# Kernel tuning notes

Hardware: AMD Instinct MI355X
Metric: run time of the kernel (lower is better)

## Reference

```python
import jax, jax.numpy as jnp
import numpy as np

D_MODEL = 1024
N_QK = 32
D_QK = 32
N_OV = 2048
D_OV = 1
SEQ = 1024
BATCH = 2
VKV = 16
ROT_DIM = 32
ROT_BASE = 10000.0
SCALE = D_QK ** 0.5  # cfg.attn_scale default = sqrt(d_qk_head)


def _kaiming(k, shape, fan_in):
    # torch kaiming_normal_(mode='fan_in', nonlinearity='relu'): std = sqrt(2/fan_in)
    return jax.random.normal(k, shape, jnp.float32) * np.sqrt(2.0 / fan_in)


def setup_inputs() -> dict:
    key = jax.random.key(0)
    ks = jax.random.split(key, 7)
    return {
        'resid': jax.random.normal(ks[0], (BATCH, SEQ, D_MODEL), jnp.float32),
        'W_Q': _kaiming(ks[1], (N_QK, D_MODEL, D_QK), D_MODEL * D_QK),
        'W_K': _kaiming(ks[2], (N_QK, D_MODEL, D_QK), D_MODEL * D_QK),
        'W_V': _kaiming(ks[3], (N_OV, D_MODEL, D_OV), D_MODEL * D_OV),
        'W_O': _kaiming(ks[4], (N_OV, D_OV, D_MODEL), D_OV * D_MODEL),
        'b_Q': jnp.zeros((N_QK, D_QK), jnp.float32),
        'b_K': jnp.zeros((N_QK, D_QK), jnp.float32),
        'b_V': jnp.zeros((N_OV, D_OV), jnp.float32),
        'virtual_k': _kaiming(ks[5], (VKV, N_QK, D_QK), N_QK * D_QK),
        'virtual_v': jnp.zeros((VKV, N_OV, D_OV), jnp.float32),
    }


def _rotary_sin_cos(n_ctx, rd, base):
    # GPT-NeoX style (non-adjacent pairs): freq repeated as (2 d)
    pos = jnp.arange(n_ctx, dtype=jnp.float32)
    dim = jnp.arange(rd // 2, dtype=jnp.float32)
    freq = base ** (dim / (rd / 2))
    freq = jnp.concatenate([freq, freq])
    angles = pos[:, None] / freq[None, :]  # (n_ctx, rd)
    return jnp.sin(angles), jnp.cos(angles)


def _apply_rotary(x, sin, cos, rd):
    # x: (batch, seq, head, d_head)
    s = x.shape[1]
    x_rot, x_pass = x[..., :rd], x[..., rd:]
    flip = jnp.concatenate([-x_rot[..., rd // 2:], x_rot[..., :rd // 2]], axis=-1)
    rot = x_rot * cos[None, :s, None, :] + flip * sin[None, :s, None, :]
    return jnp.concatenate([rot, x_pass], axis=-1)


def reference(resid, W_Q, W_K, W_V, W_O, b_Q, b_K, b_V, virtual_k, virtual_v):
    b, s, _ = resid.shape
    # per-head QKV projections + biases
    q = jnp.einsum('bsm,hmd->bshd', resid, W_Q) + b_Q  # (b,s,n_qk,d_qk)
    k = jnp.einsum('bsm,hmd->bshd', resid, W_K) + b_K
    v = jnp.einsum('bsm,hmd->bshd', resid, W_V) + b_V  # (b,s,n_ov,d_ov)
    sin, cos = _rotary_sin_cos(s, ROT_DIM, ROT_BASE)
    q = _apply_rotary(q, sin, cos, ROT_DIM)
    k = _apply_rotary(k, sin, cos, ROT_DIM)
    # append virtual KV at the end of the key axis
    k = jnp.concatenate([k, jnp.broadcast_to(virtual_k[None], (b,) + virtual_k.shape)], axis=1)
    v = jnp.concatenate([v, jnp.broadcast_to(virtual_v[None], (b,) + virtual_v.shape)], axis=1)
    kv_len = s + VKV
    scores = jnp.einsum('bqhd,bkhd->bhqk', q, k) / SCALE
    # causal mask: tril(ones(n_ctx, n_ctx+vkv), diagonal=vkv)
    mask = jnp.arange(kv_len)[None, :] <= (jnp.arange(s)[:, None] + VKV)
    scores = jnp.where(mask[None, None], scores, -jnp.inf)
    pattern = jax.nn.softmax(scores, axis=-1)
    pattern = jnp.where(jnp.isnan(pattern), 0.0, pattern)
    # repeat_interleave of pattern over ov heads == grouping v per qk head
    ratio = N_OV // N_QK
    v_g = v.reshape(b, kv_len, N_QK, ratio * D_OV)
    z = jnp.einsum('bhqk,bkhr->bqhr', pattern, v_g)  # (b,s,n_qk,ratio*d_ov)
    z = z.reshape(b, s, N_OV, D_OV)
    out = jnp.einsum('bqhd,hdm->bqm', z, W_O)  # cal_out: no b_O
    return out
```

## Files before the change

kernel.cpp:

```cpp
#include <hip/hip_runtime.h>
#include <hip/hip_bf16.h>
#include <math.h>


typedef short bf16x8 __attribute__((ext_vector_type(8)));
typedef short short4v __attribute__((ext_vector_type(4)));
typedef float f32x4 __attribute__((ext_vector_type(4)));
typedef int int4v __attribute__((ext_vector_type(4)));
typedef __hip_bfloat16 bf16;

#define AS1(p) ((const __attribute__((address_space(1))) void*)(const void*)(p))
#define AS3(p) ((__attribute__((address_space(3))) void*)(void*)(p))

static constexpr float INV_SCALE = 0.17677669529663687f;

__device__ inline short rnd_bf16(float x) {
  unsigned u = __float_as_uint(x);
  return (short)((u + 0x7fffu + ((u >> 16) & 1u)) >> 16);
}

__device__ inline int pack_bf16_pair(float hi, float lo) {
  unsigned a = __float_as_uint(hi) + 0x8000u;
  unsigned b = __float_as_uint(lo) + 0x8000u;
  return (int)__builtin_amdgcn_perm(a, b, 0x07060302u);
}

__global__ __launch_bounds__(256) void prep(
    const float* __restrict__ resid, const float* __restrict__ WV,
    const float* __restrict__ WQ, const float* __restrict__ WK,
    const float* __restrict__ WO, const float* __restrict__ vk,
    const float* __restrict__ vv,
    bf16* __restrict__ A_bf, bf16* __restrict__ Wt, bf16* __restrict__ Wot,
    bf16* __restrict__ Kb, bf16* __restrict__ Vb) {
  __shared__ float t[64][65];
  const int blk = blockIdx.x, tid = threadIdx.x;
  if (blk < 4096) {
    const float* src = (blk < 2048) ? resid : WV;
    short* dst = (short*)((blk < 2048) ? A_bf : (Wt + (size_t)2048 * 1024));
    int i = ((blk & 2047) * 256 + tid) * 4;
    float4 v = *(const float4*)(src + i);
    dst[i + 0] = rnd_bf16(v.x); dst[i + 1] = rnd_bf16(v.y);
    dst[i + 2] = rnd_bf16(v.z); dst[i + 3] = rnd_bf16(v.w);
  } else if (blk < 7168) {
    int idx = (blk - 4096) * 256 + tid;
    if (idx < 262144) {
      int b = idx >> 17, rem = idx & 131071;
      int j = rem >> 10, c = rem & 1023;
      int h = c >> 5, d = c & 31;
      float v = (j < 16) ? vk[j * 1024 + c] : 0.f;
      Kb[(((size_t)(b * 32 + h)) * 1152 + 1024 + j) * 32 + d] = __float2bfloat16(v);
    } else if (idx < 524288) {
      int i2 = idx - 262144;
      int b = i2 >> 17, rem = i2 & 131071;
      int ch = rem >> 6, p = rem & 63;
      int pl = p & 31;
      int u = (p & 32) | ((pl & 4) << 2) | ((pl & 24) >> 1) | (pl & 3);
      float v = (u < 16) ? vv[(size_t)u * 2048 + ch] : 0.f;
      int hv = ch >> 6, c = ch & 63;
      int slot = c * 8 + ((p >> 3) ^ (c & 7));
      Vb[((((size_t)(b * 32 + hv)) * 17 + 16) * 512 + slot) * 8 + (p & 7)] = __float2bfloat16(v);
    }
  } else if (blk < 8192) {
    int i = blk - 7168;
    int mt = i & 15, h = (i >> 4) & 31, qk = i >> 9;
    const float* W = qk ? WK : WQ;
    const int m0 = mt * 64;
    for (int idx = tid; idx < 64 * 32; idx += 256) {
      int ii = idx >> 5, d = idx & 31;
      t[ii][d] = W[((size_t)h * 1024 + m0 + ii) * 32 + d];
    }
    __syncthreads();
    const int rowbase = qk * 1024 + h * 32;
    for (int idx = tid; idx < 32 * 64; idx += 256) {
      int d = idx >> 6, ii = idx & 63;
      Wt[(size_t)(rowbase + d) * 1024 + m0 + ii] = __float2bfloat16(t[ii][d]);
    }
  } else {
    int i = blk - 8192;
    int h0 = (i & 31) * 64, m0 = (i >> 5) * 64;
    for (int idx = tid; idx < 64 * 64; idx += 256) {
      int ii = idx >> 6, j = idx & 63;
      t[ii][j] = WO[(size_t)(h0 + ii) * 1024 + m0 + j];
    }
    __syncthreads();
    for (int idx = tid; idx < 64 * 64; idx += 256) {
      int ii = idx >> 6, j = idx & 63;
      Wot[(size_t)(m0 + ii) * 2048 + h0 + j] = __float2bfloat16(t[j][ii]);
    }
  }
}

__global__ __launch_bounds__(256) void gemm1_fused(
    const bf16* __restrict__ A, const bf16* __restrict__ Bt,
    const float* __restrict__ bQ, const float* __restrict__ bK,
    const float* __restrict__ bV,
    bf16* __restrict__ Qb, bf16* __restrict__ Kb, bf16* __restrict__ Vb) {
  __shared__ __align__(16) short As[128 * 64];
  __shared__ __align__(16) short Bs[128 * 64];
  const int flat = blockIdx.x;
  const int xcd = flat & 7, idx = flat >> 3;
  const int tileM = (xcd * 2 + (idx >> 5)) * 128;
  const int tileN = (idx & 31) * 128;
  const int tid = threadIdx.x, wave = tid >> 6, lane = tid & 63;
  const int wm = (wave >> 1) * 64, wn = (wave & 1) * 64;
  const int mrow = lane & 15, kq = lane >> 4;
  const bool isQK = tileN < 2048;
  f32x4 acc[4][4] = {};

  for (int k0 = 0; k0 < 1024; k0 += 64) {
#pragma unroll
    for (int i = 0; i < 4; i++) {
      int c = (wave * 4 + i) * 64 + lane;
      int row = c >> 3, j = c & 7, g = j ^ (row & 7);
      const short* ga = (const short*)A + (size_t)(tileM + row) * 1024 + k0 + g * 8;
      const short* gb = (const short*)Bt + (size_t)(tileN + row) * 1024 + k0 + g * 8;
      __builtin_amdgcn_global_load_lds(AS1(ga), AS3(&As[(wave * 4 + i) * 512]), 16, 0, 0);
      __builtin_amdgcn_global_load_lds(AS1(gb), AS3(&Bs[(wave * 4 + i) * 512]), 16, 0, 0);
    }
    __syncthreads();
#pragma unroll
    for (int ks = 0; ks < 2; ks++) {
      bf16x8 af[4], bfr[4];
#pragma unroll
      for (int t = 0; t < 4; t++) {
        int ra = wm + t * 16 + mrow, rb = wn + t * 16 + mrow;
        af[t]  = *(const bf16x8*)&As[ra * 64 + ((ks * 4 + kq) ^ (ra & 7)) * 8];
        bfr[t] = *(const bf16x8*)&Bs[rb * 64 + ((ks * 4 + kq) ^ (rb & 7)) * 8];
      }
      if (isQK) {
#pragma unroll
        for (int fj = 0; fj < 4; fj++)
#pragma unroll
          for (int ti = 0; ti < 4; ti++)
            acc[fj][ti] = __builtin_amdgcn_mfma_f32_16x16x32_bf16(bfr[fj], af[ti], acc[fj][ti], 0, 0, 0);
      } else {
#pragma unroll
        for (int i = 0; i < 4; i++)
#pragma unroll
          for (int j = 0; j < 4; j++)
            acc[i][j] = __builtin_amdgcn_mfma_f32_16x16x32_bf16(af[i], bfr[j], acc[i][j], 0, 0, 0);
      }
    }
    __syncthreads();
  }

  const int col = lane & 15, rq = lane >> 4;
  if (isQK) {
    const int qk = tileN >> 10;
    const float* bias = qk ? bK : bQ;
    const int hA = ((tileN & 1023) + wn) >> 5;
    const int d0 = rq * 4;
    const float4 bA0 = *(const float4*)&bias[hA * 32 + d0];
    const float4 bA1 = *(const float4*)&bias[hA * 32 + 16 + d0];
    const float4 bB0 = *(const float4*)&bias[(hA + 1) * 32 + d0];
    const float4 bB1 = *(const float4*)&bias[(hA + 1) * 32 + 16 + d0];
    float invf[4];
#pragma unroll
    for (int r = 0; r < 4; r++)
      invf[r] = exp2f((d0 + r) * -0.8304820237218406f);
    const float osc = qk ? 1.f : INV_SCALE;
#pragma unroll
    for (int ti = 0; ti < 4; ti++) {
      int sg = tileM + wm + ti * 16 + col;
      int s = sg & 1023, bb = sg >> 10;
      float sv[4], cv[4];
#pragma unroll
      for (int r = 0; r < 4; r++) __sincosf((float)s * invf[r], &sv[r], &cv[r]);
#pragma unroll
      for (int p = 0; p < 2; p++) {
        int h = hA + p;
        short4v z0, z1;
#pragma unroll
        for (int r = 0; r < 4; r++) {
          float x0 = acc[2 * p][ti][r]     + (p ? (&bB0.x)[r] : (&bA0.x)[r]);
          float x1 = acc[2 * p + 1][ti][r] + (p ? (&bB1.x)[r] : (&bA1.x)[r]);
          float y0 = (x0 * cv[r] - x1 * sv[r]) * osc;
          float y1 = (x1 * cv[r] + x0 * sv[r]) * osc;
          z0[r] = rnd_bf16(y0); z1[r] = rnd_bf16(y1);
        }
        short* dst = qk
            ? (short*)Kb + ((size_t)(bb * 32 + h) * 1152 + s) * 32
            : (short*)Qb + ((size_t)(bb * 32 + h) * 1024 + s) * 32;
        *(short4v*)(dst + d0) = z0;
        *(short4v*)(dst + 16 + d0) = z1;
      }
    }
  } else {
    const int hv = (tileN - 2048 + wn) >> 6;
#pragma unroll
    for (int i = 0; i < 4; i++)
#pragma unroll
      for (int j = 0; j < 4; j++) {
        int c = j * 16 + col;
        float bias = bV[hv * 64 + c];
        int m0 = tileM + wm + i * 16 + rq * 4;
        int s0 = m0 & 1023, bb = m0 >> 10;
        int chunk = s0 >> 6, w = s0 & 63, u0 = w & 31;
        int p0 = (u0 & 3) | ((u0 & 16) >> 2) | ((u0 & 8) << 1) | ((u0 & 4) << 1);
        int p = (w & 32) | p0;
        int slot = c * 8 + ((p >> 3) ^ (c & 7));
        short4v s4;
#pragma unroll
        for (int r = 0; r < 4; r++) s4[r] = rnd_bf16(acc[i][j][r] + bias);
        *(short4v*)((short*)Vb +
            ((((size_t)(bb * 32 + hv)) * 17 + chunk) * 512 + slot) * 8 + (p & 7)) = s4;
      }
  }
}

__global__ __launch_bounds__(256) void attn_mfma(
    const bf16* __restrict__ Qb, const bf16* __restrict__ Kb,
    const bf16* __restrict__ Vb, bf16* __restrict__ Zb) {
  __shared__ __align__(16) short Vs[4][2][4096];
  const int flat = blockIdx.x;
  const int xcd = flat & 7;
  const int hqb = xcd * 8 + ((flat >> 3) & 7);
  const int xblk = flat >> 6;
  const int hq = hqb & 31, b = hqb >> 5;
  const int wave = threadIdx.x >> 6, lane = threadIdx.x & 63;
  const int col = lane & 15, quad = lane >> 4;
  const int pairIdx = xblk * 4 + wave;
  const int qwA = pairIdx * 16, qwB = (63 - pairIdx) * 16;

  const short* qbase = (const short*)Qb + ((size_t)(b * 32 + hq)) * 1024 * 32;
  const bf16x8 qfA = *(const bf16x8*)(qbase + (qwA + col) * 32 + quad * 8);
  const bf16x8 qfB = *(const bf16x8*)(qbase + (qwB + col) * 32 + quad * 8);
  const short* kbase = (const short*)Kb + ((size_t)(b * 32 + hq)) * 1152 * 32 + quad * 8;
  const short* vbh = (const short*)Vb + ((size_t)(b * 32 + hq)) * (17 * 4096) + lane * 8;

  const int kendA = qwA + 32;
  const int nchA = (kendA + 63) >> 6;
  const int kendB = (qwB + 32 < 1040) ? qwB + 32 : 1040;
  const int nchB = (kendB + 63) >> 6;

  f32x4 OA[4] = {}, OB[4] = {};
  float mA = -1e30f, lA = 0.f, mB = -1e30f, lB = 0.f;

  bf16x8 kf[4];
#pragma unroll
  for (int mbk = 0; mbk < 4; mbk++)
    kf[mbk] = *(const bf16x8*)(kbase + (size_t)(mbk * 16 + col) * 32);
  {
    short* vd = &Vs[wave][0][0];
#pragma unroll
    for (int g = 0; g < 8; g++)
      __builtin_amdgcn_global_load_lds(AS1(vbh + g * 512), AS3(vd + g * 512), 16, 0, 0);
  }

  for (int ci = 0; ci < nchB; ci++) {
    const int kc = ci * 64;
    const bool aAct = ci < nchA;
    f32x4 SB[4] = {};
#pragma unroll
    for (int mbk = 0; mbk < 4; mbk++)
      SB[mbk] = __builtin_amdgcn_mfma_f32_16x16x32_bf16(kf[mbk], qfB, SB[mbk], 0, 0, 0);
    f32x4 SA[4] = {};
    if (aAct) {
#pragma unroll
      for (int mbk = 0; mbk < 4; mbk++)
        SA[mbk] = __builtin_amdgcn_mfma_f32_16x16x32_bf16(kf[mbk], qfA, SA[mbk], 0, 0, 0);
    }
    if (kc + 63 > qwB + 16) {
      int qv = qwB + col + 16;
#pragma unroll
      for (int mbk = 0; mbk < 4; mbk++)
#pragma unroll
        for (int r = 0; r < 4; r++)
          if (kc + mbk * 16 + quad * 4 + r > qv) SB[mbk][r] = -1e30f;
    }
    if (aAct && kc + 63 > qwA + 16) {
      int qv = qwA + col + 16;
#pragma unroll
      for (int mbk = 0; mbk < 4; mbk++)
#pragma unroll
        for (int r = 0; r < 4; r++)
          if (kc + mbk * 16 + quad * 4 + r > qv) SA[mbk][r] = -1e30f;
    }
    int4v piB[2], piA[2];
    {
      float c0 = fmaxf(fmaxf(SB[0][0], SB[0][1]), fmaxf(SB[0][2], SB[0][3]));
      float c1 = fmaxf(fmaxf(SB[1][0], SB[1][1]), fmaxf(SB[1][2], SB[1][3]));
      float c2 = fmaxf(fmaxf(SB[2][0], SB[2][1]), fmaxf(SB[2][2], SB[2][3]));
      float c3 = fmaxf(fmaxf(SB[3][0], SB[3][1]), fmaxf(SB[3][2], SB[3][3]));
      float cmax = fmaxf(fmaxf(c0, c1), fmaxf(c2, c3));
      cmax = fmaxf(cmax, __shfl_xor(cmax, 16));
      cmax = fmaxf(cmax, __shfl_xor(cmax, 32));
      float mn = fmaxf(mB, cmax);
      float al = __expf(mB - mn);
      mB = mn;
      float ps = 0.f;
#pragma unroll
      for (int mbk = 0; mbk < 4; mbk++)
#pragma unroll
        for (int r = 0; r < 4; r++) {
          float p = __expf(SB[mbk][r] - mn);
          ps += p;
          SB[mbk][r] = p;
        }
      ps += __shfl_xor(ps, 16);
      ps += __shfl_xor(ps, 32);
      lB = lB * al + ps;
#pragma unroll
      for (int pr = 0; pr < 2; pr++)
#pragma unroll
        for (int d = 0; d < 4; d++)
          piB[pr][d] = pack_bf16_pair(SB[2 * pr + (d >> 1)][(d & 1) * 2 + 1],
                                      SB[2 * pr + (d >> 1)][(d & 1) * 2]);
#pragma unroll
      for (int cb = 0; cb < 4; cb++)
#pragma unroll
        for (int r = 0; r < 4; r++) OB[cb][r] *= al;
    }
    if (aAct) {
      float c0 = fmaxf(fmaxf(SA[0][0], SA[0][1]), fmaxf(SA[0][2], SA[0][3]));
      float c1 = fmaxf(fmaxf(SA[1][0], SA[1][1]), fmaxf(SA[1][2], SA[1][3]));
      float c2 = fmaxf(fmaxf(SA[2][0], SA[2][1]), fmaxf(SA[2][2], SA[2][3]));
      float c3 = fmaxf(fmaxf(SA[3][0], SA[3][1]), fmaxf(SA[3][2], SA[3][3]));
      float cmax = fmaxf(fmaxf(c0, c1), fmaxf(c2, c3));
      cmax = fmaxf(cmax, __shfl_xor(cmax, 16));
      cmax = fmaxf(cmax, __shfl_xor(cmax, 32));
      float mn = fmaxf(mA, cmax);
      float al = __expf(mA - mn);
      mA = mn;
      float ps = 0.f;
#pragma unroll
      for (int mbk = 0; mbk < 4; mbk++)
#pragma unroll
        for (int r = 0; r < 4; r++) {
          float p = __expf(SA[mbk][r] - mn);
          ps += p;
          SA[mbk][r] = p;
        }
      ps += __shfl_xor(ps, 16);
      ps += __shfl_xor(ps, 32);
      lA = lA * al + ps;
#pragma unroll
      for (int pr = 0; pr < 2; pr++)
#pragma unroll
        for (int d = 0; d < 4; d++)
          piA[pr][d] = pack_bf16_pair(SA[2 * pr + (d >> 1)][(d & 1) * 2 + 1],
                                      SA[2 * pr + (d >> 1)][(d & 1) * 2]);
#pragma unroll
      for (int cb = 0; cb < 4; cb++)
#pragma unroll
        for (int r = 0; r < 4; r++) OA[cb][r] *= al;
    }
    asm volatile("s_waitcnt vmcnt(0)" ::: "memory");
    const short* vd = &Vs[wave][ci & 1][0];
    bf16x8 vf[2][4];
#pragma unroll
    for (int ks = 0; ks < 2; ks++)
#pragma unroll
      for (int cb = 0; cb < 4; cb++) {
        int slot = (cb * 16 + col) * 8 + ((ks * 4 + quad) ^ (col & 7));
        vf[ks][cb] = *(const bf16x8*)(vd + slot * 8);
      }
    if (ci + 1 < nchB) {
      const int kn = kc + 64;
#pragma unroll
      for (int mbk = 0; mbk < 4; mbk++)
        kf[mbk] = *(const bf16x8*)(kbase + (size_t)(kn + mbk * 16 + col) * 32);
      const short* vsrc = vbh + (ci + 1) * 4096;
      short* vdn = &Vs[wave][(ci + 1) & 1][0];
#pragma unroll
      for (int g = 0; g < 8; g++)
        __builtin_amdgcn_global_load_lds(AS1(vsrc + g * 512), AS3(vdn + g * 512), 16, 0, 0);
    }
#pragma unroll
    for (int ks = 0; ks < 2; ks++) {
      bf16x8 prB = *(bf16x8*)&piB[ks];
#pragma unroll
      for (int cb = 0; cb < 4; cb++)
        OB[cb] = __builtin_amdgcn_mfma_f32_16x16x32_bf16(vf[ks][cb], prB, OB[cb], 0, 0, 0);
    }
    if (aAct) {
#pragma unroll
      for (int ks = 0; ks < 2; ks++) {
        bf16x8 prA = *(bf16x8*)&piA[ks];
#pragma unroll
        for (int cb = 0; cb < 4; cb++)
          OA[cb] = __builtin_amdgcn_mfma_f32_16x16x32_bf16(vf[ks][cb], prA, OA[cb], 0, 0, 0);
      }
    }
  }
  {
    float inv = 1.f / lA;
    short* zrow = (short*)Zb + ((size_t)(b * 1024 + qwA + col)) * 2048 + hq * 64 + quad * 4;
#pragma unroll
    for (int cb = 0; cb < 4; cb++) {
      short4v s4;
#pragma unroll
      for (int r = 0; r < 4; r++) s4[r] = rnd_bf16(OA[cb][r] * inv);
      *(short4v*)(zrow + cb * 16) = s4;
    }
  }
  {
    float inv = 1.f / lB;
    short* zrow = (short*)Zb + ((size_t)(b * 1024 + qwB + col)) * 2048 + hq * 64 + quad * 4;
#pragma unroll
    for (int cb = 0; cb < 4; cb++) {
      short4v s4;
#pragma unroll
      for (int r = 0; r < 4; r++) s4[r] = rnd_bf16(OB[cb][r] * inv);
      *(short4v*)(zrow + cb * 16) = s4;
    }
  }
}

__global__ __launch_bounds__(256) void gemm2_small(
    const bf16* __restrict__ A, const bf16* __restrict__ Bt, float* __restrict__ C,
    int K, int ldc) {
  __shared__ __align__(16) short As[64 * 128];
  __shared__ __align__(16) short Bs[64 * 128];
  const int tileM = blockIdx.y * 64, tileN = blockIdx.x * 64;
  const int tid = threadIdx.x, wave = tid >> 6, lane = tid & 63;
  const int wm = (wave >> 1) * 32, wn = (wave & 1) * 32;
  const int mrow = lane & 15, kq = lane >> 4;
  f32x4 acc[2][2] = {};

  for (int k0 = 0; k0 < K; k0 += 128) {
#pragma unroll
    for (int i = 0; i < 4; i++) {
      int c = (wave * 4 + i) * 64 + lane;
      int row = c >> 4, j = c & 15, g = j ^ (row & 15);
      const short* ga = (const short*)A + (size_t)(tileM + row) * K + k0 + g * 8;
      const short* gb = (const short*)Bt + (size_t)(tileN + row) * K + k0 + g * 8;
      __builtin_amdgcn_global_load_lds(AS1(ga), AS3(&As[(wave * 4 + i) * 512]), 16, 0, 0);
      __builtin_amdgcn_global_load_lds(AS1(gb), AS3(&Bs[(wave * 4 + i) * 512]), 16, 0, 0);
    }
    __syncthreads();
#pragma unroll
    for (int ks = 0; ks < 4; ks++) {
      bf16x8 af[2], bfr[2];
#pragma unroll
      for (int t = 0; t < 2; t++) {
        int ra = wm + t * 16 + mrow, rb = wn + t * 16 + mrow;
        af[t]  = *(const bf16x8*)&As[ra * 128 + ((ks * 4 + kq) ^ (ra & 15)) * 8];
        bfr[t] = *(const bf16x8*)&Bs[rb * 128 + ((ks * 4 + kq) ^ (rb & 15)) * 8];
      }
#pragma unroll
      for (int i = 0; i < 2; i++)
#pragma unroll
        for (int j = 0; j < 2; j++)
          acc[i][j] = __builtin_amdgcn_mfma_f32_16x16x32_bf16(af[i], bfr[j], acc[i][j], 0, 0, 0);
    }
    __syncthreads();
  }
  const int col = lane & 15, rq = lane >> 4;
#pragma unroll
  for (int i = 0; i < 2; i++)
#pragma unroll
    for (int j = 0; j < 2; j++)
#pragma unroll
      for (int r = 0; r < 4; r++) {
        int mm = tileM + wm + i * 16 + rq * 4 + r;
        int nn = tileN + wn + j * 16 + col;
        C[(size_t)mm * ldc + nn] = acc[i][j][r];
      }
}

extern "C" void kernel_launch(void* const* d_in, const int* in_sizes, int n_in,
                              void* d_out, int out_size, void* d_ws, size_t ws_size,
                              hipStream_t stream) {
  const float* resid = (const float*)d_in[0];
  const float* WQ = (const float*)d_in[1];
  const float* WK = (const float*)d_in[2];
  const float* WV = (const float*)d_in[3];
  const float* WO = (const float*)d_in[4];
  const float* bQ = (const float*)d_in[5];
  const float* bK = (const float*)d_in[6];
  const float* bV = (const float*)d_in[7];
  const float* vk = (const float*)d_in[8];
  const float* vv = (const float*)d_in[9];
  float* out = (float*)d_out;

  char* ws = (char*)d_ws;
  bf16* A_bf = (bf16*)(ws);
  bf16* Wt   = (bf16*)(ws + 4194304);
  bf16* Wot  = (bf16*)(ws + 12582912);
  bf16* Qb   = (bf16*)(ws + 16777216);
  bf16* Kb   = (bf16*)(ws + 20971520);
  bf16* Vb   = (bf16*)(ws + 25690112);
  bf16* Zb   = (bf16*)(ws + 35127296);

  prep<<<8704, 256, 0, stream>>>(resid, WV, WQ, WK, WO, vk, vv, A_bf, Wt, Wot, Kb, Vb);
  gemm1_fused<<<512, 256, 0, stream>>>(A_bf, Wt, bQ, bK, bV, Qb, Kb, Vb);
  attn_mfma<<<512, 256, 0, stream>>>(Qb, Kb, Vb, Zb);
  gemm2_small<<<dim3(16, 32), 256, 0, stream>>>(Zb, Wot, out, 2048, 1024);
}
```

Measured before the change: 160.1 us.

## Double-buffer LDS tiles in output GEMM and reorder attention block scheduling

The output-projection GEMM now keeps two LDS buffers, so the global-to-LDS loads for the next K tile are issued before the MFMA work on the current tile. This is meant to hide global memory latency behind compute, at the cost of doubling LDS use, which may lower occupancy. Separately, the attention kernel remaps block indices above 3 in reverse order, changing which query-pair blocks are dispatched together to balance the causal workload.

```diff
diff --git a/kernel.cpp b/kernel.cpp
--- a/kernel.cpp
+++ b/kernel.cpp
@@ -215,7 +215,8 @@
   const int flat = blockIdx.x;
   const int xcd = flat & 7;
   const int hqb = xcd * 8 + ((flat >> 3) & 7);
-  const int xblk = flat >> 6;
+  const int xb = flat >> 6;
+  const int xblk = (xb < 4) ? xb : (11 - xb);
   const int hq = hqb & 31, b = hqb >> 5;
   const int wave = threadIdx.x >> 6, lane = threadIdx.x & 63;
   const int col = lane & 15, quad = lane >> 4;
@@ -410,33 +411,45 @@
 __global__ __launch_bounds__(256) void gemm2_small(
     const bf16* __restrict__ A, const bf16* __restrict__ Bt, float* __restrict__ C,
     int K, int ldc) {
-  __shared__ __align__(16) short As[64 * 128];
-  __shared__ __align__(16) short Bs[64 * 128];
+  __shared__ __align__(16) short As[2][64 * 128];
+  __shared__ __align__(16) short Bs[2][64 * 128];
   const int tileM = blockIdx.y * 64, tileN = blockIdx.x * 64;
   const int tid = threadIdx.x, wave = tid >> 6, lane = tid & 63;
   const int wm = (wave >> 1) * 32, wn = (wave & 1) * 32;
   const int mrow = lane & 15, kq = lane >> 4;
   f32x4 acc[2][2] = {};
 
-  for (int k0 = 0; k0 < K; k0 += 128) {
-#pragma unroll
-    for (int i = 0; i < 4; i++) {
-      int c = (wave * 4 + i) * 64 + lane;
-      int row = c >> 4, j = c & 15, g = j ^ (row & 15);
-      const short* ga = (const short*)A + (size_t)(tileM + row) * K + k0 + g * 8;
-      const short* gb = (const short*)Bt + (size_t)(tileN + row) * K + k0 + g * 8;
-      __builtin_amdgcn_global_load_lds(AS1(ga), AS3(&As[(wave * 4 + i) * 512]), 16, 0, 0);
-      __builtin_amdgcn_global_load_lds(AS1(gb), AS3(&Bs[(wave * 4 + i) * 512]), 16, 0, 0);
-    }
-    __syncthreads();
+  const int cbase = wave * 4;
+  const int nt = K >> 7;
+
+#define G2_STAGE(buf, k0)                                                     \
+  {                                                                           \
+    _Pragma("unroll")                                                         \
+    for (int i = 0; i < 4; i++) {                                             \
+      int c = (cbase + i) * 64 + lane;                                        \
+      int row = c >> 4, j = c & 15, g = j ^ (row & 15);                       \
+      const short* ga = (const short*)A + (size_t)(tileM + row) * K + (k0) + g * 8; \
+      const short* gb = (const short*)Bt + (size_t)(tileN + row) * K + (k0) + g * 8; \
+      __builtin_amdgcn_global_load_lds(AS1(ga), AS3(&As[buf][(cbase + i) * 512]), 16, 0, 0); \
+      __builtin_amdgcn_global_load_lds(AS1(gb), AS3(&Bs[buf][(cbase + i) * 512]), 16, 0, 0); \
+    }                                                                         \
+  }
+
+  G2_STAGE(0, 0);
+  __syncthreads();
+  int cur = 0;
+  for (int t = 0; t < nt; ++t) {
+    if (t + 1 < nt) G2_STAGE(cur ^ 1, (t + 1) << 7);
+    const short* as = &As[cur][0];
+    const short* bs = &Bs[cur][0];
 #pragma unroll
     for (int ks = 0; ks < 4; ks++) {
       bf16x8 af[2], bfr[2];
 #pragma unroll
-      for (int t = 0; t < 2; t++) {
-        int ra = wm + t * 16 + mrow, rb = wn + t * 16 + mrow;
-        af[t]  = *(const bf16x8*)&As[ra * 128 + ((ks * 4 + kq) ^ (ra & 15)) * 8];
-        bfr[t] = *(const bf16x8*)&Bs[rb * 128 + ((ks * 4 + kq) ^ (rb & 15)) * 8];
+      for (int t2 = 0; t2 < 2; t2++) {
+        int ra = wm + t2 * 16 + mrow, rb = wn + t2 * 16 + mrow;
+        af[t2]  = *(const bf16x8*)&as[ra * 128 + ((ks * 4 + kq) ^ (ra & 15)) * 8];
+        bfr[t2] = *(const bf16x8*)&bs[rb * 128 + ((ks * 4 + kq) ^ (rb & 15)) * 8];
       }
 #pragma unroll
       for (int i = 0; i < 2; i++)
@@ -445,7 +458,10 @@
           acc[i][j] = __builtin_amdgcn_mfma_f32_16x16x32_bf16(af[i], bfr[j], acc[i][j], 0, 0, 0);
     }
     __syncthreads();
-  }
+    cur ^= 1;
+  }
+#undef G2_STAGE
+
   const int col = lane & 15, rq = lane >> 4;
 #pragma unroll
   for (int i = 0; i < 2; i++)
```

Result: no change. 159.6 us (-0.3%).
